# Kernel tuning notes

Measured on AMD Instinct MI355X. Metric: run time of the kernel, lower is better.

## Reference

```python
import jax, jax.numpy as jnp
import numpy as np
import math

B, S, D_MODEL, N_HEAD = 4, 2048, 1024, 16
D_K = D_MODEL // N_HEAD
ROPE_THETA = 10000.0


def _rope(x):
    # x: [B, H, S, Dk]; interleaved-pair rotary embedding.
    b, h, s, d = x.shape
    inv_freq = ROPE_THETA ** (-jnp.arange(0, d, 2, dtype=jnp.float32) / d)  # [d/2]
    ang = jnp.arange(s, dtype=jnp.float32)[:, None] * inv_freq[None, :]      # [S, d/2]
    cos, sin = jnp.cos(ang), jnp.sin(ang)
    x1, x2 = x[..., 0::2], x[..., 1::2]
    r1 = x1 * cos - x2 * sin
    r2 = x1 * sin + x2 * cos
    return jnp.stack([r1, r2], axis=-1).reshape(b, h, s, d)


def setup_inputs() -> dict:
    key = jax.random.key(0)
    ks = jax.random.split(key, 7)
    sc = 1.0 / math.sqrt(D_MODEL)
    return {
        "q": jax.random.normal(ks[0], (B, S, D_MODEL), jnp.float32),
        "k": jax.random.normal(ks[1], (B, S, D_MODEL), jnp.float32),
        "v": jax.random.normal(ks[2], (B, S, D_MODEL), jnp.float32),
        "Wq": jax.random.normal(ks[3], (D_MODEL, D_MODEL), jnp.float32) * sc,
        "Wk": jax.random.normal(ks[4], (D_MODEL, D_MODEL), jnp.float32) * sc,
        "Wv": jax.random.normal(ks[5], (D_MODEL, D_MODEL), jnp.float32) * sc,
        "Wo": jax.random.normal(ks[6], (D_MODEL, D_MODEL), jnp.float32) * sc,
    }


def _split(x):
    b, s, d = x.shape
    return x.reshape(b, s, N_HEAD, d // N_HEAD).transpose(0, 2, 1, 3)  # [B,H,S,Dk]


def reference(q, k, v, Wq, Wk, Wv, Wo):
    q = jnp.einsum("bsd,de->bse", q, Wq)
    k = jnp.einsum("bsd,de->bse", k, Wk)
    v = jnp.einsum("bsd,de->bse", v, Wv)
    qh, kh, vh = _split(q), _split(k), _split(v)
    qh, kh = _rope(qh), _rope(kh)
    scale = 1.0 / math.sqrt(D_K)
    score = jnp.einsum("bhqd,bhkd->bhqk", qh, kh) * scale  # [B,H,S,S]
    attn = jax.nn.softmax(score, axis=-1)
    out = jnp.einsum("bhqk,bhkd->bhqd", attn, vh)
    out = out.transpose(0, 2, 1, 3).reshape(q.shape[0], q.shape[1], D_MODEL)
    return jnp.einsum("bsd,de->bse", out, Wo)
```

## Files before the change

kernel.cpp:

```cpp
#include <hip/hip_runtime.h>
#include <stdint.h>

#define Bv 4
#define Sv 2048
#define Dv 1024
#define Hv 16
#define DKv 64
#define BSv (Bv * Sv)

typedef unsigned short u16;
typedef __attribute__((ext_vector_type(8))) short short8;
typedef __attribute__((ext_vector_type(8))) unsigned short u16x8;
typedef __attribute__((ext_vector_type(4))) unsigned short u16x4;
typedef __attribute__((ext_vector_type(4))) float f32x4;
typedef __attribute__((ext_vector_type(16))) float f32x16;

__device__ __forceinline__ u16 f2bf(float f) {
  union { float f; uint32_t u; } x; x.f = f;
  uint32_t r = x.u + 0x7FFFu + ((x.u >> 16) & 1u);
  return (u16)(r >> 16);
}

__device__ __forceinline__ void gl_lds16(const void* g, void* l) {
  __builtin_amdgcn_global_load_lds(
      (__attribute__((address_space(1))) void*)g,
      (__attribute__((address_space(3))) void*)l, 16, 0, 0);
}

__device__ __forceinline__ f32x4 mfma16(short8 a, short8 b, f32x4 c) {
  return __builtin_amdgcn_mfma_f32_16x16x32_bf16(a, b, c, 0, 0, 0);
}
__device__ __forceinline__ f32x16 mfma32(short8 a, short8 b, f32x16 c) {
  return __builtin_amdgcn_mfma_f32_32x32x16_bf16(a, b, c, 0, 0, 0);
}

template <int N>
__device__ __forceinline__ void vwait() {
  asm volatile("s_waitcnt vmcnt(%0)" ::"n"(N) : "memory");
}
__device__ __forceinline__ void bar() {
  asm volatile("" ::: "memory");
  __builtin_amdgcn_s_barrier();
  asm volatile("" ::: "memory");
}

__global__ __launch_bounds__(256) void conv_wt(
    const float* __restrict__ w0, const float* __restrict__ w1,
    const float* __restrict__ w2, const float* __restrict__ w3,
    u16* __restrict__ t0, u16* __restrict__ t1, u16* __restrict__ t2,
    u16* __restrict__ t3) {
  const float* W = (blockIdx.z == 0) ? w0 : (blockIdx.z == 1 ? w1 : (blockIdx.z == 2 ? w2 : w3));
  u16* T = (blockIdx.z == 0) ? t0 : (blockIdx.z == 1 ? t1 : (blockIdx.z == 2 ? t2 : t3));
  __shared__ u16 tile[64][72];
  int nb = blockIdx.x * 64, kb = blockIdx.y * 64;
  int t = threadIdx.x;
#pragma unroll
  for (int p = 0; p < 4; ++p) {
    int idx = p * 256 + t;
    int r = idx >> 4;
    int c4 = (idx & 15) * 4;
    float4 vv = *(const float4*)(W + (size_t)(kb + r) * Dv + nb + c4);
    tile[c4 + 0][r] = f2bf(vv.x);
    tile[c4 + 1][r] = f2bf(vv.y);
    tile[c4 + 2][r] = f2bf(vv.z);
    tile[c4 + 3][r] = f2bf(vv.w);
  }
  __syncthreads();
#pragma unroll
  for (int p = 0; p < 4; ++p) {
    int idx = p * 256 + t;
    int r = idx >> 4;
    int c4 = (idx & 15) * 4;
    u16x4 o = { tile[r][c4], tile[r][c4 + 1], tile[r][c4 + 2], tile[r][c4 + 3] };
    *(u16x4*)(T + (size_t)(nb + r) * Dv + kb + c4) = o;
  }
}

__global__ __launch_bounds__(256, 2) void gemm_qkv(
    const float* __restrict__ A0, const float* __restrict__ A1, const float* __restrict__ A2,
    const u16* __restrict__ B0, const u16* __restrict__ B1, const u16* __restrict__ B2,
    u16* __restrict__ O0, u16* __restrict__ O1, u16* __restrict__ O2) {
  __shared__ u16 As[2][128 * 64];
  __shared__ u16 Bs[2][128 * 64];
  int z = blockIdx.z;
  const float* A = (z == 0) ? A0 : (z == 1 ? A1 : A2);
  const u16* Bt  = (z == 0) ? B0 : (z == 1 ? B1 : B2);
  u16* Out       = (z == 0) ? O0 : (z == 1 ? O1 : O2);
  int mode = z;

  int tid = threadIdx.x;
  int lane = tid & 63, wid = tid >> 6;
  int quad = lane >> 4, cc = lane & 15;
  int wm = (wid >> 1) * 64, wn = (wid & 1) * 64;
  int m0 = blockIdx.x * 128, n0 = blockIdx.y * 128;

  f32x4 acc[4][4];
#pragma unroll
  for (int mi = 0; mi < 4; ++mi)
#pragma unroll
    for (int ni = 0; ni < 4; ++ni) {
      f32x4 zf = {0.f, 0.f, 0.f, 0.f};
      acc[mi][ni] = zf;
    }

  auto stageB = [&](int ki, int b) {
#pragma unroll
    for (int p = 0; p < 4; ++p) {
      int slot = p * 256 + tid;
      int row = slot >> 3, cl = slot & 7;
      int cg = cl ^ (row & 7);
      gl_lds16(Bt + (size_t)(n0 + row) * Dv + ki * 64 + cg * 8, &Bs[b][slot * 8]);
    }
  };

  float4 fa[4][2];
  auto loadA = [&](int ki) {
#pragma unroll
    for (int p = 0; p < 4; ++p) {
      int slot = p * 256 + tid;
      int row = slot >> 3, cl = slot & 7;
      int cg = cl ^ (row & 7);
      const float* g = A + (size_t)(m0 + row) * Dv + ki * 64 + cg * 8;
      fa[p][0] = *(const float4*)g;
      fa[p][1] = *(const float4*)(g + 4);
    }
  };
  auto writeA = [&](int b) {
#pragma unroll
    for (int p = 0; p < 4; ++p) {
      int slot = p * 256 + tid;
      u16x8 o = { f2bf(fa[p][0].x), f2bf(fa[p][0].y), f2bf(fa[p][0].z), f2bf(fa[p][0].w),
                  f2bf(fa[p][1].x), f2bf(fa[p][1].y), f2bf(fa[p][1].z), f2bf(fa[p][1].w) };
      *(u16x8*)&As[b][slot * 8] = o;
    }
  };

  loadA(0); writeA(0); stageB(0, 0);

  const int NT = Dv / 64;
  for (int t = 0; t < NT; ++t) {
    int cur = t & 1;
    __syncthreads();

    if (t + 1 < NT) {
      stageB(t + 1, 1 - cur);
      loadA(t + 1);
    }

#pragma unroll
    for (int kk = 0; kk < 2; ++kk) {
      short8 af[4], bfr[4];
#pragma unroll
      for (int mi = 0; mi < 4; ++mi) {
        int row = wm + mi * 16 + cc;
        int cg = kk * 4 + quad;
        af[mi] = *(const short8*)&As[cur][row * 64 + (cg ^ (row & 7)) * 8];
      }
#pragma unroll
      for (int ni = 0; ni < 4; ++ni) {
        int row = wn + ni * 16 + cc;
        int cg = kk * 4 + quad;
        bfr[ni] = *(const short8*)&Bs[cur][row * 64 + (cg ^ (row & 7)) * 8];
      }
#pragma unroll
      for (int mi = 0; mi < 4; ++mi)
#pragma unroll
        for (int ni = 0; ni < 4; ++ni)
          acc[mi][ni] = mfma16(af[mi], bfr[ni], acc[mi][ni]);
    }

    if (t + 1 < NT) writeA(1 - cur);
  }

  if (mode <= 1) {
    float postscale = (mode == 0) ? 0.18033688011112042f : 1.0f;
#pragma unroll
    for (int ni = 0; ni < 4; ++ni) {
      int n = n0 + wn + ni * 16 + cc;
      int h = n >> 6, d = n & 63;
      float inv = __expf(-(float)(d & 62) * (9.210340372f / 64.0f));
      float sign = (d & 1) ? 1.0f : -1.0f;
#pragma unroll
      for (int mi = 0; mi < 4; ++mi) {
        int mB = m0 + wm + mi * 16 + quad * 4;
#pragma unroll
        for (int r = 0; r < 4; ++r) {
          int m = mB + r;
          int b = m >> 11, s = m & (Sv - 1);
          float val = acc[mi][ni][r];
          float part = __shfl_xor(val, 1);
          float sn, cs;
          __sincosf((float)s * inv, &sn, &cs);
          float outv = (val * cs + sign * part * sn) * postscale;
          Out[((size_t)(b * Hv + h) * Sv + s) * DKv + d] = f2bf(outv);
        }
      }
    }
  } else {
#pragma unroll
    for (int ni = 0; ni < 4; ++ni) {
      int n = n0 + wn + ni * 16 + cc;
      int h = n >> 6, d = n & 63;
#pragma unroll
      for (int mi = 0; mi < 4; ++mi) {
        int mB = m0 + wm + mi * 16 + quad * 4;
        int b = mB >> 11, s = mB & (Sv - 1);
        u16x4 o4 = { f2bf(acc[mi][ni][0]), f2bf(acc[mi][ni][1]),
                     f2bf(acc[mi][ni][2]), f2bf(acc[mi][ni][3]) };
        *(u16x4*)&Out[((size_t)(b * Hv + h) * DKv + d) * Sv + s] = o4;
      }
    }
  }
}

__global__ __launch_bounds__(512, 2) void gemm_bt(
    const u16* __restrict__ A0, const u16* __restrict__ A1, const u16* __restrict__ A2,
    const u16* __restrict__ B0, const u16* __restrict__ B1, const u16* __restrict__ B2,
    void* __restrict__ O0, void* __restrict__ O1, void* __restrict__ O2,
    int modeSel) {
  __shared__ u16 As[3][256 * 64];
  __shared__ u16 Bs[3][128 * 64];
  int z = blockIdx.z;
  const u16* A  = (z == 0) ? A0 : (z == 1 ? A1 : A2);
  const u16* Bt = (z == 0) ? B0 : (z == 1 ? B1 : B2);
  void* Out     = (z == 0) ? O0 : (z == 1 ? O1 : O2);
  int mode = (modeSel < 0) ? z : modeSel;

  int tid = threadIdx.x;
  int lane = tid & 63, wid = tid >> 6;
  int quad = lane >> 4, cc = lane & 15;
  int wm = (wid >> 1) * 64, wn = (wid & 1) * 64;
  int bx = blockIdx.x;
  int swz = (bx & 7) * 32 + (bx >> 3);
  int m0 = (swz >> 3) * 256, n0 = (swz & 7) * 128;

  f32x4 acc[4][4];
#pragma unroll
  for (int mi = 0; mi < 4; ++mi)
#pragma unroll
    for (int ni = 0; ni < 4; ++ni) {
      f32x4 zf = {0.f, 0.f, 0.f, 0.f};
      acc[mi][ni] = zf;
    }

  auto stageA2 = [&](int ki, int b, int p0) {
#pragma unroll
    for (int p = 0; p < 2; ++p) {
      int slot = (p0 + p) * 512 + tid;
      int row = slot >> 3, cl = slot & 7;
      int cg = cl ^ (row & 7);
      gl_lds16(A + (size_t)(m0 + row) * Dv + ki * 64 + cg * 8, &As[b][slot * 8]);
    }
  };
  auto stageB1 = [&](int ki, int b, int p0) {
    int slot = p0 * 512 + tid;
    int row = slot >> 3, cl = slot & 7;
    int cg = cl ^ (row & 7);
    gl_lds16(Bt + (size_t)(n0 + row) * Dv + ki * 64 + cg * 8, &Bs[b][slot * 8]);
  };

  stageA2(0, 0, 0); stageA2(0, 0, 2); stageB1(0, 0, 0); stageB1(0, 0, 1);
  stageA2(1, 1, 0); stageA2(1, 1, 2); stageB1(1, 1, 0); stageB1(1, 1, 1);
  vwait<6>();
  bar();

  const int NT = Dv / 64;
  int cur = 0, nxt = 2;
#pragma unroll 1
  for (int t = 0; t < NT; ++t) {
    const u16* Ac = &As[cur][0];
    const u16* Bc = &Bs[cur][0];
#pragma unroll
    for (int kk = 0; kk < 2; ++kk) {
      short8 af[4], bfr[4];
#pragma unroll
      for (int mi = 0; mi < 4; ++mi) {
        int row = wm + mi * 16 + cc;
        int cg = kk * 4 + quad;
        af[mi] = *(const short8*)&Ac[row * 64 + (cg ^ (row & 7)) * 8];
      }
#pragma unroll
      for (int ni = 0; ni < 4; ++ni) {
        int row = wn + ni * 16 + cc;
        int cg = kk * 4 + quad;
        bfr[ni] = *(const short8*)&Bc[row * 64 + (cg ^ (row & 7)) * 8];
      }
      if (t + 2 < NT) {
        if (kk == 0) { stageA2(t + 2, nxt, 0); stageB1(t + 2, nxt, 0); }
        else         { stageA2(t + 2, nxt, 2); stageB1(t + 2, nxt, 1); }
      }
      bar();
      __builtin_amdgcn_s_setprio(1);
#pragma unroll
      for (int mi = 0; mi < 4; ++mi)
#pragma unroll
        for (int ni = 0; ni < 4; ++ni)
          acc[mi][ni] = mfma16(af[mi], bfr[ni], acc[mi][ni]);
      __builtin_amdgcn_s_setprio(0);
      if (kk == 0) bar();
    }
    if (t < NT - 1) {
      if (t + 2 < NT) vwait<6>(); else vwait<0>();
      bar();
    }
    cur = (cur == 2) ? 0 : cur + 1;
    nxt = (nxt == 2) ? 0 : nxt + 1;
  }

  if (mode <= 1) {
    u16* O = (u16*)Out;
    float postscale = (mode == 0) ? 0.18033688011112042f : 1.0f;
#pragma unroll
    for (int ni = 0; ni < 4; ++ni) {
      int n = n0 + wn + ni * 16 + cc;
      int h = n >> 6, d = n & 63;
      float inv = __expf(-(float)(d & 62) * (9.210340372f / 64.0f));
      float sign = (d & 1) ? 1.0f : -1.0f;
#pragma unroll
      for (int mi = 0; mi < 4; ++mi) {
        int mB = m0 + wm + mi * 16 + quad * 4;
#pragma unroll
        for (int r = 0; r < 4; ++r) {
          int m = mB + r;
          int b = m >> 11, s = m & (Sv - 1);
          float val = acc[mi][ni][r];
          float part = __shfl_xor(val, 1);
          float sn, cs;
          __sincosf((float)s * inv, &sn, &cs);
          float outv = (val * cs + sign * part * sn) * postscale;
          O[((size_t)(b * Hv + h) * Sv + s) * DKv + d] = f2bf(outv);
        }
      }
    }
  } else if (mode == 2) {
    u16* O = (u16*)Out;
#pragma unroll
    for (int ni = 0; ni < 4; ++ni) {
      int n = n0 + wn + ni * 16 + cc;
      int h = n >> 6, d = n & 63;
#pragma unroll
      for (int mi = 0; mi < 4; ++mi) {
        int mB = m0 + wm + mi * 16 + quad * 4;
        int b = mB >> 11, s = mB & (Sv - 1);
        u16x4 o4 = { f2bf(acc[mi][ni][0]), f2bf(acc[mi][ni][1]),
                     f2bf(acc[mi][ni][2]), f2bf(acc[mi][ni][3]) };
        *(u16x4*)&O[((size_t)(b * Hv + h) * DKv + d) * Sv + s] = o4;
      }
    }
  } else {
    float* O = (float*)Out;
#pragma unroll
    for (int ni = 0; ni < 4; ++ni) {
      int n = n0 + wn + ni * 16 + cc;
#pragma unroll
      for (int mi = 0; mi < 4; ++mi) {
        int mB = m0 + wm + mi * 16 + quad * 4;
#pragma unroll
        for (int r = 0; r < 4; ++r)
          O[(size_t)(mB + r) * Dv + n] = acc[mi][ni][r];
      }
    }
  }
}

__global__ __launch_bounds__(256, 4) void attn(
    const u16* __restrict__ Qp, const u16* __restrict__ Kp,
    const u16* __restrict__ Vt, u16* __restrict__ ctx) {
  __shared__ u16 Ks[2][64 * 64];
  __shared__ u16 Vs[2][64 * 64];
  int tid = threadIdx.x;
  int lane = tid & 63, wid = tid >> 6;
  int hi = lane >> 5, c32 = lane & 31;
  int sz = (c32 & 7) ^ ((c32 >> 3) & 3);
  int bx = blockIdx.x;
  int u = (bx & 7) * 128 + (bx >> 3);
  int bh = u >> 4;
  int q0 = (u & 15) * 128 + wid * 32;
  const u16* Qh = Qp + (size_t)bh * Sv * DKv;
  const u16* Kh = Kp + (size_t)bh * Sv * DKv;
  const u16* Vh = Vt + (size_t)bh * Sv * DKv;

  const short8 ones = { (short)0x3F80, (short)0x3F80, (short)0x3F80, (short)0x3F80,
                        (short)0x3F80, (short)0x3F80, (short)0x3F80, (short)0x3F80 };

  short8 qf[4];
#pragma unroll
  for (int dk = 0; dk < 4; ++dk)
    qf[dk] = *(const short8*)&Qh[(size_t)(q0 + c32) * DKv + dk * 16 + hi * 8];

  f32x16 o[2];
  f32x16 ol;
#pragma unroll
  for (int dt = 0; dt < 2; ++dt)
#pragma unroll
    for (int r = 0; r < 16; ++r) o[dt][r] = 0.f;
#pragma unroll
  for (int r = 0; r < 16; ++r) ol[r] = 0.f;

#pragma unroll
  for (int p = 0; p < 2; ++p) {
    int slot = p * 256 + tid;
    int row = slot >> 3, cl = slot & 7;
    int cg = cl ^ ((row & 7) ^ ((row >> 3) & 3));
    gl_lds16(Kh + (size_t)row * DKv + cg * 8, &Ks[0][slot * 8]);
    gl_lds16(Vh + (size_t)row * Sv + cg * 8, &Vs[0][slot * 8]);
  }

  for (int kt = 0; kt < Sv / 64; ++kt) {
    int cur = kt & 1;
    __syncthreads();

    if (kt + 1 < Sv / 64) {
      int s1 = (kt + 1) * 64;
#pragma unroll
      for (int p = 0; p < 2; ++p) {
        int slot = p * 256 + tid;
        int row = slot >> 3, cl = slot & 7;
        int cg = cl ^ ((row & 7) ^ ((row >> 3) & 3));
        gl_lds16(Kh + (size_t)(s1 + row) * DKv + cg * 8, &Ks[1 - cur][slot * 8]);
        gl_lds16(Vh + (size_t)row * Sv + s1 + cg * 8, &Vs[1 - cur][slot * 8]);
      }
    }

#pragma unroll
    for (int half = 0; half < 2; ++half) {
      short8 kf[4];
#pragma unroll
      for (int dk = 0; dk < 4; ++dk)
        kf[dk] = *(const short8*)&Ks[cur][(half * 32 + c32) * 64 + (((dk * 2 + hi) ^ sz)) * 8];

      f32x16 st;
#pragma unroll
      for (int r = 0; r < 16; ++r) st[r] = 0.f;
#pragma unroll
      for (int dk = 0; dk < 4; ++dk)
        st = mfma32(kf[dk], qf[dk], st);

#pragma unroll
      for (int pp = 0; pp < 2; ++pp) {
        int pk = half * 2 + pp;
        short8 vf[2];
#pragma unroll
        for (int dt = 0; dt < 2; ++dt)
          vf[dt] = *(const short8*)&Vs[cur][(dt * 32 + c32) * 64 + (((pk * 2 + hi) ^ sz)) * 8];
        float e0 = __builtin_amdgcn_exp2f(st[8 * pp + 0]);
        float e1 = __builtin_amdgcn_exp2f(st[8 * pp + 1]);
        float e2 = __builtin_amdgcn_exp2f(st[8 * pp + 2]);
        float e3 = __builtin_amdgcn_exp2f(st[8 * pp + 3]);
        float e4 = __builtin_amdgcn_exp2f(st[8 * pp + 4]);
        float e5 = __builtin_amdgcn_exp2f(st[8 * pp + 5]);
        float e6 = __builtin_amdgcn_exp2f(st[8 * pp + 6]);
        float e7 = __builtin_amdgcn_exp2f(st[8 * pp + 7]);
        uint32_t plo0 = __builtin_amdgcn_perm(__float_as_uint(e1), __float_as_uint(e0), 0x07060302u);
        uint32_t plo1 = __builtin_amdgcn_perm(__float_as_uint(e3), __float_as_uint(e2), 0x07060302u);
        uint32_t phi0 = __builtin_amdgcn_perm(__float_as_uint(e5), __float_as_uint(e4), 0x07060302u);
        uint32_t phi1 = __builtin_amdgcn_perm(__float_as_uint(e7), __float_as_uint(e6), 0x07060302u);
        uint32_t s0 = hi ? plo0 : phi0;
        uint32_t s1 = hi ? plo1 : phi1;
        uint32_t r0 = (uint32_t)__shfl_xor((int)s0, 32);
        uint32_t r1 = (uint32_t)__shfl_xor((int)s1, 32);
        union { uint32_t u[4]; short8 s8; } pu;
        pu.u[0] = hi ? r0 : plo0;
        pu.u[1] = hi ? r1 : plo1;
        pu.u[2] = hi ? phi0 : r0;
        pu.u[3] = hi ? phi1 : r1;
        ol = mfma32(pu.s8, ones, ol);
        o[0] = mfma32(pu.s8, vf[0], o[0]);
        o[1] = mfma32(pu.s8, vf[1], o[1]);
      }
    }
  }

  int b = bh >> 4, h = bh & 15;
#pragma unroll
  for (int r = 0; r < 16; ++r) {
    int q = q0 + (r & 3) + 8 * (r >> 2) + 4 * hi;
    float linv = 1.0f / ol[r];
#pragma unroll
    for (int dt = 0; dt < 2; ++dt) {
      int d = h * DKv + dt * 32 + c32;
      ctx[((size_t)b * Sv + q) * Dv + d] = f2bf(o[dt][r] * linv);
    }
  }
}

extern "C" void kernel_launch(void* const* d_in, const int* in_sizes, int n_in,
                              void* d_out, int out_size, void* d_ws, size_t ws_size,
                              hipStream_t stream) {
  (void)in_sizes; (void)n_in; (void)out_size; (void)ws_size;
  const float* q  = (const float*)d_in[0];
  const float* k  = (const float*)d_in[1];
  const float* v  = (const float*)d_in[2];
  const float* Wq = (const float*)d_in[3];
  const float* Wk = (const float*)d_in[4];
  const float* Wv = (const float*)d_in[5];
  const float* Wo = (const float*)d_in[6];

  char* ws = (char*)d_ws;
  size_t off = 0;
  const size_t big = (size_t)BSv * Dv * sizeof(u16);
  const size_t wsz = (size_t)Dv * Dv * sizeof(u16);
  u16* Wqt = (u16*)(ws + off); off += wsz;
  u16* Wkt = (u16*)(ws + off); off += wsz;
  u16* Wvt = (u16*)(ws + off); off += wsz;
  u16* Wot = (u16*)(ws + off); off += wsz;
  u16* Qp  = (u16*)(ws + off); off += big;
  u16* Kp  = (u16*)(ws + off); off += big;
  u16* Vtr = (u16*)(ws + off); off += big;
  u16* ctx = (u16*)(ws + off); off += big;

  conv_wt<<<dim3(Dv / 64, Dv / 64, 4), 256, 0, stream>>>(Wq, Wk, Wv, Wo, Wqt, Wkt, Wvt, Wot);
  gemm_qkv<<<dim3(BSv / 128, Dv / 128, 3), 256, 0, stream>>>(
      q, k, v, Wqt, Wkt, Wvt, Qp, Kp, Vtr);
  attn<<<dim3(Sv / 128 * Bv * Hv), 256, 0, stream>>>(Qp, Kp, Vtr, ctx);
  gemm_bt<<<dim3(256, 1, 1), 512, 0, stream>>>(
      ctx, ctx, ctx, Wot, Wot, Wot, d_out, d_out, d_out, 3);
}
```

Measured before the change: 343.6 us.

## Double query rows per attention wave and prefetch GEMM A tiles two steps ahead

```diff
diff --git a/kernel.cpp b/kernel.cpp
--- a/kernel.cpp
+++ b/kernel.cpp
@@ -113,39 +113,38 @@
     }
   };
 
-  float4 fa[4][2];
-  auto loadA = [&](int ki) {
+  float4 fa[2][4][2];
+  auto loadA = [&](int ki, int s) {
 #pragma unroll
     for (int p = 0; p < 4; ++p) {
       int slot = p * 256 + tid;
       int row = slot >> 3, cl = slot & 7;
       int cg = cl ^ (row & 7);
       const float* g = A + (size_t)(m0 + row) * Dv + ki * 64 + cg * 8;
-      fa[p][0] = *(const float4*)g;
-      fa[p][1] = *(const float4*)(g + 4);
+      fa[s][p][0] = *(const float4*)g;
+      fa[s][p][1] = *(const float4*)(g + 4);
     }
   };
-  auto writeA = [&](int b) {
+  auto writeA = [&](int b, int s) {
 #pragma unroll
     for (int p = 0; p < 4; ++p) {
       int slot = p * 256 + tid;
-      u16x8 o = { f2bf(fa[p][0].x), f2bf(fa[p][0].y), f2bf(fa[p][0].z), f2bf(fa[p][0].w),
-                  f2bf(fa[p][1].x), f2bf(fa[p][1].y), f2bf(fa[p][1].z), f2bf(fa[p][1].w) };
+      u16x8 o = { f2bf(fa[s][p][0].x), f2bf(fa[s][p][0].y), f2bf(fa[s][p][0].z), f2bf(fa[s][p][0].w),
+                  f2bf(fa[s][p][1].x), f2bf(fa[s][p][1].y), f2bf(fa[s][p][1].z), f2bf(fa[s][p][1].w) };
       *(u16x8*)&As[b][slot * 8] = o;
     }
   };
 
-  loadA(0); writeA(0); stageB(0, 0);
+  loadA(0, 0); writeA(0, 0); stageB(0, 0);
+  loadA(1, 1);
 
   const int NT = Dv / 64;
   for (int t = 0; t < NT; ++t) {
     int cur = t & 1;
     __syncthreads();
 
-    if (t + 1 < NT) {
-      stageB(t + 1, 1 - cur);
-      loadA(t + 1);
-    }
+    if (t + 1 < NT) stageB(t + 1, 1 - cur);
+    if (t + 2 < NT) loadA(t + 2, cur);
 
 #pragma unroll
     for (int kk = 0; kk < 2; ++kk) {
@@ -169,7 +168,7 @@
           acc[mi][ni] = mfma16(af[mi], bfr[ni], acc[mi][ni]);
     }
 
-    if (t + 1 < NT) writeA(1 - cur);
+    if (t + 1 < NT) writeA(1 - cur, 1 - cur);
   }
 
   if (mode <= 1) {
@@ -363,7 +362,7 @@
   }
 }
 
-__global__ __launch_bounds__(256, 4) void attn(
+__global__ __launch_bounds__(256, 2) void attn(
     const u16* __restrict__ Qp, const u16* __restrict__ Kp,
     const u16* __restrict__ Vt, u16* __restrict__ ctx) {
   __shared__ u16 Ks[2][64 * 64];
@@ -372,10 +371,8 @@
   int lane = tid & 63, wid = tid >> 6;
   int hi = lane >> 5, c32 = lane & 31;
   int sz = (c32 & 7) ^ ((c32 >> 3) & 3);
-  int bx = blockIdx.x;
-  int u = (bx & 7) * 128 + (bx >> 3);
-  int bh = u >> 4;
-  int q0 = (u & 15) * 128 + wid * 32;
+  int bh = blockIdx.y;
+  int q0 = blockIdx.x * 256 + wid * 64;
   const u16* Qh = Qp + (size_t)bh * Sv * DKv;
   const u16* Kh = Kp + (size_t)bh * Sv * DKv;
   const u16* Vh = Vt + (size_t)bh * Sv * DKv;
@@ -383,19 +380,24 @@
   const short8 ones = { (short)0x3F80, (short)0x3F80, (short)0x3F80, (short)0x3F80,
                         (short)0x3F80, (short)0x3F80, (short)0x3F80, (short)0x3F80 };
 
-  short8 qf[4];
-#pragma unroll
-  for (int dk = 0; dk < 4; ++dk)
-    qf[dk] = *(const short8*)&Qh[(size_t)(q0 + c32) * DKv + dk * 16 + hi * 8];
-
-  f32x16 o[2];
-  f32x16 ol;
-#pragma unroll
-  for (int dt = 0; dt < 2; ++dt)
-#pragma unroll
-    for (int r = 0; r < 16; ++r) o[dt][r] = 0.f;
-#pragma unroll
-  for (int r = 0; r < 16; ++r) ol[r] = 0.f;
+  short8 qf[2][4];
+#pragma unroll
+  for (int qs = 0; qs < 2; ++qs)
+#pragma unroll
+    for (int dk = 0; dk < 4; ++dk)
+      qf[qs][dk] = *(const short8*)&Qh[(size_t)(q0 + qs * 32 + c32) * DKv + dk * 16 + hi * 8];
+
+  f32x16 o[2][2];
+  f32x16 ol[2];
+#pragma unroll
+  for (int qs = 0; qs < 2; ++qs) {
+#pragma unroll
+    for (int dt = 0; dt < 2; ++dt)
+#pragma unroll
+      for (int r = 0; r < 16; ++r) o[qs][dt][r] = 0.f;
+#pragma unroll
+    for (int r = 0; r < 16; ++r) ol[qs][r] = 0.f;
+  }
 
 #pragma unroll
   for (int p = 0; p < 2; ++p) {
@@ -429,12 +431,15 @@
       for (int dk = 0; dk < 4; ++dk)
         kf[dk] = *(const short8*)&Ks[cur][(half * 32 + c32) * 64 + (((dk * 2 + hi) ^ sz)) * 8];
 
-      f32x16 st;
-#pragma unroll
-      for (int r = 0; r < 16; ++r) st[r] = 0.f;
-#pragma unroll
-      for (int dk = 0; dk < 4; ++dk)
-        st = mfma32(kf[dk], qf[dk], st);
+      f32x16 st[2];
+#pragma unroll
+      for (int qs = 0; qs < 2; ++qs) {
+#pragma unroll
+        for (int r = 0; r < 16; ++r) st[qs][r] = 0.f;
+#pragma unroll
+        for (int dk = 0; dk < 4; ++dk)
+          st[qs] = mfma32(kf[dk], qf[qs][dk], st[qs]);
+      }
 
 #pragma unroll
       for (int pp = 0; pp < 2; ++pp) {
@@ -443,45 +448,50 @@
 #pragma unroll
         for (int dt = 0; dt < 2; ++dt)
           vf[dt] = *(const short8*)&Vs[cur][(dt * 32 + c32) * 64 + (((pk * 2 + hi) ^ sz)) * 8];
-        float e0 = __builtin_amdgcn_exp2f(st[8 * pp + 0]);
-        float e1 = __builtin_amdgcn_exp2f(st[8 * pp + 1]);
-        float e2 = __builtin_amdgcn_exp2f(st[8 * pp + 2]);
-        float e3 = __builtin_amdgcn_exp2f(st[8 * pp + 3]);
-        float e4 = __builtin_amdgcn_exp2f(st[8 * pp + 4]);
-        float e5 = __builtin_amdgcn_exp2f(st[8 * pp + 5]);
-        float e6 = __builtin_amdgcn_exp2f(st[8 * pp + 6]);
-        float e7 = __builtin_amdgcn_exp2f(st[8 * pp + 7]);
-        uint32_t plo0 = __builtin_amdgcn_perm(__float_as_uint(e1), __float_as_uint(e0), 0x07060302u);
-        uint32_t plo1 = __builtin_amdgcn_perm(__float_as_uint(e3), __float_as_uint(e2), 0x07060302u);
-        uint32_t phi0 = __builtin_amdgcn_perm(__float_as_uint(e5), __float_as_uint(e4), 0x07060302u);
-        uint32_t phi1 = __builtin_amdgcn_perm(__float_as_uint(e7), __float_as_uint(e6), 0x07060302u);
-        uint32_t s0 = hi ? plo0 : phi0;
-        uint32_t s1 = hi ? plo1 : phi1;
-        uint32_t r0 = (uint32_t)__shfl_xor((int)s0, 32);
-        uint32_t r1 = (uint32_t)__shfl_xor((int)s1, 32);
-        union { uint32_t u[4]; short8 s8; } pu;
-        pu.u[0] = hi ? r0 : plo0;
-        pu.u[1] = hi ? r1 : plo1;
-        pu.u[2] = hi ? phi0 : r0;
-        pu.u[3] = hi ? phi1 : r1;
-        ol = mfma32(pu.s8, ones, ol);
-        o[0] = mfma32(pu.s8, vf[0], o[0]);
-        o[1] = mfma32(pu.s8, vf[1], o[1]);
+#pragma unroll
+        for (int qs = 0; qs < 2; ++qs) {
+          float e0 = __builtin_amdgcn_exp2f(st[qs][8 * pp + 0]);
+          float e1 = __builtin_amdgcn_exp2f(st[qs][8 * pp + 1]);
+          float e2 = __builtin_amdgcn_exp2f(st[qs][8 * pp + 2]);
+          float e3 = __builtin_amdgcn_exp2f(st[qs][8 * pp + 3]);
+          float e4 = __builtin_amdgcn_exp2f(st[qs][8 * pp + 4]);
+          float e5 = __builtin_amdgcn_exp2f(st[qs][8 * pp + 5]);
+          float e6 = __builtin_amdgcn_exp2f(st[qs][8 * pp + 6]);
+          float e7 = __builtin_amdgcn_exp2f(st[qs][8 * pp + 7]);
+          uint32_t plo0 = __builtin_amdgcn_perm(__float_as_uint(e1), __float_as_uint(e0), 0x07060302u);
+          uint32_t plo1 = __builtin_amdgcn_perm(__float_as_uint(e3), __float_as_uint(e2), 0x07060302u);
+          uint32_t phi0 = __builtin_amdgcn_perm(__float_as_uint(e5), __float_as_uint(e4), 0x07060302u);
+          uint32_t phi1 = __builtin_amdgcn_perm(__float_as_uint(e7), __float_as_uint(e6), 0x07060302u);
+          uint32_t s0 = hi ? plo0 : phi0;
+          uint32_t s1 = hi ? plo1 : phi1;
+          uint32_t r0 = (uint32_t)__shfl_xor((int)s0, 32);
+          uint32_t r1 = (uint32_t)__shfl_xor((int)s1, 32);
+          union { uint32_t u[4]; short8 s8; } pu;
+          pu.u[0] = hi ? r0 : plo0;
+          pu.u[1] = hi ? r1 : plo1;
+          pu.u[2] = hi ? phi0 : r0;
+          pu.u[3] = hi ? phi1 : r1;
+          ol[qs] = mfma32(pu.s8, ones, ol[qs]);
+          o[qs][0] = mfma32(pu.s8, vf[0], o[qs][0]);
+          o[qs][1] = mfma32(pu.s8, vf[1], o[qs][1]);
+        }
       }
     }
   }
 
   int b = bh >> 4, h = bh & 15;
 #pragma unroll
-  for (int r = 0; r < 16; ++r) {
-    int q = q0 + (r & 3) + 8 * (r >> 2) + 4 * hi;
-    float linv = 1.0f / ol[r];
-#pragma unroll
-    for (int dt = 0; dt < 2; ++dt) {
-      int d = h * DKv + dt * 32 + c32;
-      ctx[((size_t)b * Sv + q) * Dv + d] = f2bf(o[dt][r] * linv);
-    }
-  }
+  for (int qs = 0; qs < 2; ++qs)
+#pragma unroll
+    for (int r = 0; r < 16; ++r) {
+      int q = q0 + qs * 32 + (r & 3) + 8 * (r >> 2) + 4 * hi;
+      float linv = 1.0f / ol[qs][r];
+#pragma unroll
+      for (int dt = 0; dt < 2; ++dt) {
+        int d = h * DKv + dt * 32 + c32;
+        ctx[((size_t)b * Sv + q) * Dv + d] = f2bf(o[qs][dt][r] * linv);
+      }
+    }
 }
 
 extern "C" void kernel_launch(void* const* d_in, const int* in_sizes, int n_in,
@@ -512,7 +522,7 @@
   conv_wt<<<dim3(Dv / 64, Dv / 64, 4), 256, 0, stream>>>(Wq, Wk, Wv, Wo, Wqt, Wkt, Wvt, Wot);
   gemm_qkv<<<dim3(BSv / 128, Dv / 128, 3), 256, 0, stream>>>(
       q, k, v, Wqt, Wkt, Wvt, Qp, Kp, Vtr);
-  attn<<<dim3(Sv / 128 * Bv * Hv), 256, 0, stream>>>(Qp, Kp, Vtr, ctx);
+  attn<<<dim3(Sv / 256, Bv * Hv), 256, 0, stream>>>(Qp, Kp, Vtr, ctx);
   gemm_bt<<<dim3(256, 1, 1), 512, 0, stream>>>(
       ctx, ctx, ctx, Wot, Wot, Wot, d_out, d_out, d_out, 3);
 }
```

Measured after the change: 540.4 us. 1.57x slower.
